# Performance work log

Measured on AMD Instinct MI355X. Metric: run time of the kernel, lower is better.

The kernel has to match this reference:

```python
import jax, jax.numpy as jnp
import numpy as np

CUTOFF = 5.0
MAX_NBR = 32      # max_num_neighbors
LOOP = True
B, M = 128, 1024  # molecules, atoms per molecule (batch is uniform: batch[i] = i // M)
BOX = 26.0        # box side chosen so ~30 atoms fall within CUTOFF


def setup_inputs() -> dict:
    key = jax.random.key(0)
    pos = jax.random.uniform(key, (B * M, 3), dtype=jnp.float32) * BOX
    batch = jnp.repeat(jnp.arange(B, dtype=jnp.int32), M)
    return {"pos": pos, "batch": batch}


def reference(pos, batch):
    # radius_graph with per-graph (molecule) candidate search. Equal-size
    # molecules (batch = arange // M) let us use a dense [B, M, M] candidate
    # matrix per molecule; truncation keeps the K nearest within cutoff
    # (PyG keeps an arbitrary K within cutoff; nearest-K is the deterministic
    # variant). Output has fixed shape [2, B*M*K] padded with self-loops.
    posb = pos.reshape(B, M, 3)
    sq = jnp.sum(posb * posb, axis=-1)                       # [B, M]
    dot = jnp.einsum('bmd,bnd->bmn', posb, posb)             # [B, M, M]
    d2 = jnp.maximum(sq[:, :, None] + sq[:, None, :] - 2.0 * dot, 0.0)
    within = d2 <= CUTOFF * CUTOFF
    if not LOOP:
        within = within & ~jnp.eye(M, dtype=bool)[None]
    neg = jnp.where(within, -d2, -jnp.inf)
    vals, idx = jax.lax.top_k(neg, MAX_NBR)                  # [B, M, K]
    valid = jnp.isfinite(vals)
    center = jnp.arange(M, dtype=idx.dtype)[None, :, None]   # [1, M, 1]
    idx_eff = jnp.where(valid, idx, center)                  # pad invalid -> self

    b_ix = jnp.arange(B)[:, None, None]
    nbr = posb[b_ix, idx_eff]                                # [B, M, K, 3]
    edge_vec = nbr - posb[:, :, None, :]                     # pos[src] - pos[dst]

    is_self = idx_eff == center
    wmask = valid & ~is_self                                 # self-loops get weight 0
    d2sel = jnp.sum(edge_vec * edge_vec, axis=-1)
    edge_weight = jnp.where(wmask, jnp.sqrt(jnp.where(wmask, d2sel, 1.0)), 0.0)

    offs = (jnp.arange(B, dtype=idx.dtype) * M)[:, None, None]
    src = (offs + idx_eff).reshape(-1)                       # neighbor (edge_index[0])
    dst = jnp.broadcast_to(offs + center, (B, M, MAX_NBR)).reshape(-1)
    edge_index = jnp.stack([src, dst])                       # [2, B*M*K]
    return edge_index, edge_weight.reshape(-1), edge_vec.reshape(-1, 3)
```

## Files before the change

### kernel.cpp

```cpp
#include <hip/hip_runtime.h>

#define NB 128
#define NM 1024
#define NK 32
#define NS 16
#define CUT2 25.0f
#define CUT2_BITS 0x41C80000u
#define KEYMASK   0xFFFFFC00u

typedef unsigned int   u32;
typedef unsigned short u16;
typedef float vf4 __attribute__((ext_vector_type(4)));

__global__ __launch_bounds__(256) void pack_atoms(const float* __restrict__ pos,
                                                  float4* __restrict__ scanb)
{
  int i = blockIdx.x * 256 + threadIdx.x;
  float x = pos[3*i+0], y = pos[3*i+1], z = pos[3*i+2];
  float sq = x*x + y*y + z*z;
  scanb[i] = make_float4(-2.f*x, -2.f*y, -2.f*z, sq);
}

__device__ __forceinline__ void ce_asc(u32 &a, u32 &b) {
  u32 mn = a < b ? a : b;
  u32 mx = a < b ? b : a;
  a = mn; b = mx;
}

template <int N, int K, int D>
__device__ __forceinline__ void bitonic_pass(u32* r) {
#pragma unroll
  for (int i = 0; i < N; ++i)
    if ((i & D) == 0) {
      if ((i & K) == 0) ce_asc(r[i], r[i | D]);
      else              ce_asc(r[i | D], r[i]);
    }
}

__global__ __launch_bounds__(256, 4) void radius_knn(const float4* __restrict__ scanb,
                                                     float* __restrict__ out)
{
  __shared__ float4 s4[NM];
  __shared__ u32 lmem[4096];
  u16* lists = (u16*)lmem;

  const int tid  = threadIdx.x;
  const int lane = tid & 127;
  const int half = tid >> 7;
  const int molb = blockIdx.x & 127;
  const int q8   = blockIdx.x >> 7;
  const int c    = molb * NM + q8 * 128 + lane;
  const int mloc = c & (NM - 1);

  const float4* st = scanb + (size_t)molb * NM;
  for (int t = tid; t < NM; t += 256) s4[t] = st[t];
  __syncthreads();

  const float4 mc = s4[mloc];
  const float mex = -0.5f * mc.x, mey = -0.5f * mc.y, mez = -0.5f * mc.z;
  const float mew = mc.w;

  const float4* mp = scanb + ((size_t)(c >> 10) << 10);
  const int jbase = half * 512;
  int cnt = 0;
  float4 ta[8], tb[8];
#pragma unroll
  for (int u = 0; u < 8; ++u) ta[u] = mp[jbase + u];
  __builtin_amdgcn_sched_barrier(0);

  auto body = [&](const float4* t, int j0) {
#pragma unroll
    for (int u = 0; u < 8; ++u) {
      float d2 = __builtin_fmaf(mex, t[u].x,
                 __builtin_fmaf(mey, t[u].y,
                 __builtin_fmaf(mez, t[u].z, mew + t[u].w)));
      int slot = cnt < NS ? cnt : (NS - 1);
      lists[slot * 256 + tid] = (u16)(j0 + u);
      cnt += (d2 <= CUT2) ? 1 : 0;
    }
  };

  for (int g = 0; g < 64; g += 2) {
    const int j1 = jbase + (((g + 1) & 63) << 3);
#pragma unroll
    for (int u = 0; u < 8; ++u) tb[u] = mp[j1 + u];
    __builtin_amdgcn_sched_barrier(0);
    body(ta, jbase + (g << 3));
    const int j2 = jbase + (((g + 2) & 63) << 3);
#pragma unroll
    for (int u = 0; u < 8; ++u) ta[u] = mp[j2 + u];
    __builtin_amdgcn_sched_barrier(0);
    body(tb, jbase + ((g + 1) << 3));
  }
  if (cnt > NS) cnt = NS;

  const u32 PADK = 0x7F800000u | (u32)mloc;
  u32 r[NK];
#pragma unroll
  for (int k = 0; k < NS; ++k) {
    u32 key = PADK;
    if (k < cnt) {
      int j = lists[k * 256 + tid];
      float4 cj = s4[j];
      float d2 = fmaxf(__builtin_fmaf(mex, cj.x,
                  __builtin_fmaf(mey, cj.y,
                  __builtin_fmaf(mez, cj.z, mew + cj.w))), 0.f);
      key = (__float_as_uint(d2) & KEYMASK) | (u32)j;
    }
    r[k] = key;
  }
  bitonic_pass<16, 2, 1>(r);
  bitonic_pass<16, 4, 2>(r); bitonic_pass<16, 4, 1>(r);
  bitonic_pass<16, 8, 4>(r); bitonic_pass<16, 8, 2>(r); bitonic_pass<16, 8, 1>(r);
  bitonic_pass<16,16, 8>(r); bitonic_pass<16,16, 4>(r); bitonic_pass<16,16, 2>(r); bitonic_pass<16,16, 1>(r);

  __syncthreads();
  {
    u32* myp = lmem + half * 2048 + lane * 16;
#pragma unroll
    for (int k = 0; k < NS; ++k) myp[(k + lane) & 15] = r[k];
  }
  __syncthreads();
  {
    u32* op = lmem + (1 - half) * 2048 + lane * 16;
#pragma unroll
    for (int i = 0; i < NS; ++i) r[16 + i] = op[((15 - i) + lane) & 15];
  }
  bitonic_pass<32,32,16>(r); bitonic_pass<32,32, 8>(r); bitonic_pass<32,32, 4>(r);
  bitonic_pass<32,32, 2>(r); bitonic_pass<32,32, 1>(r);

  const long long E = (long long)NB * NM * NK;
  const float base = (float)((c >> 10) * NM);
  const float nmex = -mex, nmey = -mey, nmez = -mez;

  if (!half) {
    vf4* ps = (vf4*)(out       + (size_t)c * NK);
    vf4* pd = (vf4*)(out +   E + (size_t)c * NK);
    vf4* pw = (vf4*)(out + 2*E + (size_t)c * NK);
    const float fc = (float)c;
    const vf4 dstv = {fc, fc, fc, fc};
#pragma unroll
    for (int q = 0; q < 8; ++q) {
      float sv[4], wv[4];
#pragma unroll
      for (int u = 0; u < 4; ++u) {
        u32 key = r[4*q + u];
        int idx = (int)(key & 1023u);
        float4 cj = s4[idx];
        bool valid = (key & KEYMASK) <= CUT2_BITS;
        float vx = __builtin_fmaf(-0.5f, cj.x, nmex);
        float vy = __builtin_fmaf(-0.5f, cj.y, nmey);
        float vz = __builtin_fmaf(-0.5f, cj.z, nmez);
        bool wm  = valid && (idx != mloc);
        float d2s = vx*vx + vy*vy + vz*vz;
        wv[u] = wm ? sqrtf(d2s) : 0.0f;
        sv[u] = base + (float)idx;
      }
      ps[q] = (vf4){sv[0], sv[1], sv[2], sv[3]};
      pd[q] = dstv;
      pw[q] = (vf4){wv[0], wv[1], wv[2], wv[3]};
    }
  } else {
    vf4* pv = (vf4*)(out + 3*E + (size_t)c * NK * 3);
#pragma unroll
    for (int q = 0; q < 8; ++q) {
      float vv[12];
#pragma unroll
      for (int u = 0; u < 4; ++u) {
        int idx = (int)(r[4*q + u] & 1023u);
        float4 cj = s4[idx];
        vv[3*u+0] = __builtin_fmaf(-0.5f, cj.x, nmex);
        vv[3*u+1] = __builtin_fmaf(-0.5f, cj.y, nmey);
        vv[3*u+2] = __builtin_fmaf(-0.5f, cj.z, nmez);
      }
      pv[3*q+0] = (vf4){vv[0], vv[1], vv[2],  vv[3]};
      pv[3*q+1] = (vf4){vv[4], vv[5], vv[6],  vv[7]};
      pv[3*q+2] = (vf4){vv[8], vv[9], vv[10], vv[11]};
    }
  }
}

extern "C" void kernel_launch(void* const* d_in, const int* in_sizes, int n_in,
                              void* d_out, int out_size, void* d_ws, size_t ws_size,
                              hipStream_t stream) {
  const float* pos = (const float*)d_in[0];
  float* out = (float*)d_out;
  float4* scanb = (float4*)d_ws;
  hipLaunchKernelGGL(pack_atoms, dim3((NB*NM)/256), dim3(256), 0, stream, pos, scanb);
  hipLaunchKernelGGL(radius_knn, dim3(2*(NB*NM)/256), dim3(256), 0, stream, scanb, out);
}
```

Measured before the change: 187.2 us.

## Split each center's candidate scan across four thread quarters with two-stage merge

Each block now handles 64 centers, and four wavefront quarters each scan 256 candidates instead of two halves scanning 512. The per-thread keep list drops from 16 to 12 candidates. Partial top-K lists are merged pairwise in two rounds through LDS: first a bitonic merge, then a min-merge plus bitonic cleanup. Output writing is split four ways (indices, weights, two halves of the vectors), and the occupancy hint rises to 5 blocks. The aim is to shorten the serial scan per thread and spread the output stores, at the cost of twice as many blocks each loading the full molecule into LDS, extra syncs, and a lower per-quarter candidate cap that could drop neighbors in dense regions.

New measurement: 187.0 us. About the same (-0.1%).

```diff
diff --git a/kernel.cpp b/kernel.cpp
--- a/kernel.cpp
+++ b/kernel.cpp
@@ -3,7 +3,8 @@
 #define NB 128
 #define NM 1024
 #define NK 32
-#define NS 16
+#define NQ 4
+#define NS 12
 #define CUT2 25.0f
 #define CUT2_BITS 0x41C80000u
 #define KEYMASK   0xFFFFFC00u
@@ -37,20 +38,20 @@
     }
 }
 
-__global__ __launch_bounds__(256, 4) void radius_knn(const float4* __restrict__ scanb,
+__global__ __launch_bounds__(256, 5) void radius_knn(const float4* __restrict__ scanb,
                                                      float* __restrict__ out)
 {
   __shared__ float4 s4[NM];
   __shared__ u32 lmem[4096];
   u16* lists = (u16*)lmem;
 
-  const int tid  = threadIdx.x;
-  const int lane = tid & 127;
-  const int half = tid >> 7;
-  const int molb = blockIdx.x & 127;
-  const int q8   = blockIdx.x >> 7;
-  const int c    = molb * NM + q8 * 128 + lane;
-  const int mloc = c & (NM - 1);
+  const int tid     = threadIdx.x;
+  const int ctr     = tid & 63;
+  const int quarter = tid >> 6;
+  const int molb    = blockIdx.x & 127;
+  const int grp     = blockIdx.x >> 7;
+  const int c       = molb * NM + grp * 64 + ctr;
+  const int mloc    = c & (NM - 1);
 
   const float4* st = scanb + (size_t)molb * NM;
   for (int t = tid; t < NM; t += 256) s4[t] = st[t];
@@ -61,16 +62,16 @@
   const float mew = mc.w;
 
   const float4* mp = scanb + ((size_t)(c >> 10) << 10);
-  const int jbase = half * 512;
+  const int jbase = quarter * 256;
   int cnt = 0;
-  float4 ta[8], tb[8];
-#pragma unroll
-  for (int u = 0; u < 8; ++u) ta[u] = mp[jbase + u];
+  float4 ta[4], tb[4];
+#pragma unroll
+  for (int u = 0; u < 4; ++u) ta[u] = mp[jbase + u];
   __builtin_amdgcn_sched_barrier(0);
 
   auto body = [&](const float4* t, int j0) {
 #pragma unroll
-    for (int u = 0; u < 8; ++u) {
+    for (int u = 0; u < 4; ++u) {
       float d2 = __builtin_fmaf(mex, t[u].x,
                  __builtin_fmaf(mey, t[u].y,
                  __builtin_fmaf(mez, t[u].z, mew + t[u].w)));
@@ -81,23 +82,23 @@
   };
 
   for (int g = 0; g < 64; g += 2) {
-    const int j1 = jbase + (((g + 1) & 63) << 3);
-#pragma unroll
-    for (int u = 0; u < 8; ++u) tb[u] = mp[j1 + u];
+    const int j1 = jbase + (((g + 1) & 63) << 2);
+#pragma unroll
+    for (int u = 0; u < 4; ++u) tb[u] = mp[j1 + u];
     __builtin_amdgcn_sched_barrier(0);
-    body(ta, jbase + (g << 3));
-    const int j2 = jbase + (((g + 2) & 63) << 3);
-#pragma unroll
-    for (int u = 0; u < 8; ++u) ta[u] = mp[j2 + u];
+    body(ta, jbase + (g << 2));
+    const int j2 = jbase + (((g + 2) & 63) << 2);
+#pragma unroll
+    for (int u = 0; u < 4; ++u) ta[u] = mp[j2 + u];
     __builtin_amdgcn_sched_barrier(0);
-    body(tb, jbase + ((g + 1) << 3));
+    body(tb, jbase + ((g + 1) << 2));
   }
   if (cnt > NS) cnt = NS;
 
   const u32 PADK = 0x7F800000u | (u32)mloc;
-  u32 r[NK];
-#pragma unroll
-  for (int k = 0; k < NS; ++k) {
+  u32 r[32];
+#pragma unroll
+  for (int k = 0; k < 16; ++k) {
     u32 key = PADK;
     if (k < cnt) {
       int j = lists[k * 256 + tid];
@@ -116,15 +117,34 @@
 
   __syncthreads();
   {
-    u32* myp = lmem + half * 2048 + lane * 16;
-#pragma unroll
-    for (int k = 0; k < NS; ++k) myp[(k + lane) & 15] = r[k];
+    u32* myp = lmem + quarter * 1024 + ctr * 16;
+#pragma unroll
+    for (int k = 0; k < 16; ++k) myp[(k + ctr) & 15] = r[k];
   }
   __syncthreads();
   {
-    u32* op = lmem + (1 - half) * 2048 + lane * 16;
-#pragma unroll
-    for (int i = 0; i < NS; ++i) r[16 + i] = op[((15 - i) + lane) & 15];
+    u32* op = lmem + (quarter ^ 1) * 1024 + ctr * 16;
+#pragma unroll
+    for (int i = 0; i < 16; ++i) r[16 + i] = op[((15 - i) + ctr) & 15];
+  }
+  bitonic_pass<32,32,16>(r); bitonic_pass<32,32, 8>(r); bitonic_pass<32,32, 4>(r);
+  bitonic_pass<32,32, 2>(r); bitonic_pass<32,32, 1>(r);
+
+  __syncthreads();
+  const int pairId = quarter >> 1;
+  if ((quarter & 1) == 0) {
+    u32* pp = lmem + pairId * 2048 + ctr * 32;
+#pragma unroll
+    for (int k = 0; k < 32; ++k) pp[(k + ctr) & 31] = r[k];
+  }
+  __syncthreads();
+  {
+    u32* opp = lmem + (1 - pairId) * 2048 + ctr * 32;
+#pragma unroll
+    for (int t = 0; t < 32; ++t) {
+      u32 v = opp[((31 - t) + ctr) & 31];
+      r[t] = r[t] < v ? r[t] : v;
+    }
   }
   bitonic_pass<32,32,16>(r); bitonic_pass<32,32, 8>(r); bitonic_pass<32,32, 4>(r);
   bitonic_pass<32,32, 2>(r); bitonic_pass<32,32, 1>(r);
@@ -133,15 +153,24 @@
   const float base = (float)((c >> 10) * NM);
   const float nmex = -mex, nmey = -mey, nmez = -mez;
 
-  if (!half) {
+  if (quarter == 0) {
     vf4* ps = (vf4*)(out       + (size_t)c * NK);
     vf4* pd = (vf4*)(out +   E + (size_t)c * NK);
-    vf4* pw = (vf4*)(out + 2*E + (size_t)c * NK);
     const float fc = (float)c;
     const vf4 dstv = {fc, fc, fc, fc};
 #pragma unroll
     for (int q = 0; q < 8; ++q) {
-      float sv[4], wv[4];
+      float sv[4];
+#pragma unroll
+      for (int u = 0; u < 4; ++u) sv[u] = base + (float)(int)(r[4*q + u] & 1023u);
+      ps[q] = (vf4){sv[0], sv[1], sv[2], sv[3]};
+      pd[q] = dstv;
+    }
+  } else if (quarter == 1) {
+    vf4* pw = (vf4*)(out + 2*E + (size_t)c * NK);
+#pragma unroll
+    for (int q = 0; q < 8; ++q) {
+      float wv[4];
 #pragma unroll
       for (int u = 0; u < 4; ++u) {
         u32 key = r[4*q + u];
@@ -154,16 +183,13 @@
         bool wm  = valid && (idx != mloc);
         float d2s = vx*vx + vy*vy + vz*vz;
         wv[u] = wm ? sqrtf(d2s) : 0.0f;
-        sv[u] = base + (float)idx;
       }
-      ps[q] = (vf4){sv[0], sv[1], sv[2], sv[3]};
-      pd[q] = dstv;
       pw[q] = (vf4){wv[0], wv[1], wv[2], wv[3]};
     }
-  } else {
+  } else if (quarter == 2) {
     vf4* pv = (vf4*)(out + 3*E + (size_t)c * NK * 3);
 #pragma unroll
-    for (int q = 0; q < 8; ++q) {
+    for (int q = 0; q < 4; ++q) {
       float vv[12];
 #pragma unroll
       for (int u = 0; u < 4; ++u) {
@@ -177,6 +203,23 @@
       pv[3*q+1] = (vf4){vv[4], vv[5], vv[6],  vv[7]};
       pv[3*q+2] = (vf4){vv[8], vv[9], vv[10], vv[11]};
     }
+  } else {
+    vf4* pv = (vf4*)(out + 3*E + (size_t)c * NK * 3) + 12;
+#pragma unroll
+    for (int q = 0; q < 4; ++q) {
+      float vv[12];
+#pragma unroll
+      for (int u = 0; u < 4; ++u) {
+        int idx = (int)(r[16 + 4*q + u] & 1023u);
+        float4 cj = s4[idx];
+        vv[3*u+0] = __builtin_fmaf(-0.5f, cj.x, nmex);
+        vv[3*u+1] = __builtin_fmaf(-0.5f, cj.y, nmey);
+        vv[3*u+2] = __builtin_fmaf(-0.5f, cj.z, nmez);
+      }
+      pv[3*q+0] = (vf4){vv[0], vv[1], vv[2],  vv[3]};
+      pv[3*q+1] = (vf4){vv[4], vv[5], vv[6],  vv[7]};
+      pv[3*q+2] = (vf4){vv[8], vv[9], vv[10], vv[11]};
+    }
   }
 }
 
@@ -187,5 +230,6 @@
   float* out = (float*)d_out;
   float4* scanb = (float4*)d_ws;
   hipLaunchKernelGGL(pack_atoms, dim3((NB*NM)/256), dim3(256), 0, stream, pos, scanb);
-  hipLaunchKernelGGL(radius_knn, dim3(2*(NB*NM)/256), dim3(256), 0, stream, scanb, out);
-}
+  hipLaunchKernelGGL(radius_knn, dim3(NB * (NM / 64)), dim3(256), 0, stream,
+                     scanb, out);
+}
```
